# Optimization experiments

Hardware: AMD Instinct MI355X
Metric: run time of the kernel (lower is better)

The kernel has to match this reference:

```python
import jax, jax.numpy as jnp
import numpy as np

DIM = 2048
N_HEADS = 32
N_KV_HEADS = 8
HEAD_DIM = DIM // N_HEADS  # 64
N_REP = N_HEADS // N_KV_HEADS  # 4
B, S = 1, 2048


def _rope(t, cos, sin):
    # t: (b, s, h, head_dim); cos/sin: (s, head_dim//2)
    tr = t.reshape(*t.shape[:-1], -1, 2)
    a, b = tr[..., 0], tr[..., 1]
    c = cos[None, :, None, :]
    s_ = sin[None, :, None, :]
    ra = a * c - b * s_
    rb = a * s_ + b * c
    return jnp.stack([ra, rb], axis=-1).reshape(t.shape)


def setup_inputs() -> dict:
    key = jax.random.key(0)
    ks = jax.random.split(key, 6)
    sc = 1.0 / np.sqrt(DIM)
    x = jax.random.normal(ks[0], (B, S, DIM), dtype=jnp.float32)
    wq = jax.random.normal(ks[1], (DIM, N_HEADS * HEAD_DIM), dtype=jnp.float32) * sc
    wk = jax.random.normal(ks[2], (DIM, N_KV_HEADS * HEAD_DIM), dtype=jnp.float32) * sc
    wv = jax.random.normal(ks[3], (DIM, N_KV_HEADS * HEAD_DIM), dtype=jnp.float32) * sc
    wo = jax.random.normal(ks[4], (N_HEADS * HEAD_DIM, DIM), dtype=jnp.float32) * sc
    # rotary frequencies (theta = 500000 as in Llama3)
    inv = 1.0 / (500000.0 ** (np.arange(0, HEAD_DIM, 2, dtype=np.float32) / HEAD_DIM))
    ang = np.arange(S, dtype=np.float32)[:, None] * inv[None, :]
    freqs_cos = jnp.asarray(np.cos(ang), dtype=jnp.float32)
    freqs_sin = jnp.asarray(np.sin(ang), dtype=jnp.float32)
    # causal additive mask
    mask = jnp.triu(jnp.full((S, S), -1e9, dtype=jnp.float32), k=1)
    return {"x": x, "wq": wq, "wk": wk, "wv": wv, "wo": wo,
            "freqs_cos": freqs_cos, "freqs_sin": freqs_sin, "mask": mask,
            "start_pos": 0}


def reference(x, wq, wk, wv, wo, freqs_cos, freqs_sin, mask, start_pos):
    b, s, _ = x.shape
    xq = (x @ wq).reshape(b, s, N_HEADS, HEAD_DIM)
    xk = (x @ wk).reshape(b, s, N_KV_HEADS, HEAD_DIM)
    xv = (x @ wv).reshape(b, s, N_KV_HEADS, HEAD_DIM)
    xq = _rope(xq, freqs_cos, freqs_sin)
    xk = _rope(xk, freqs_cos, freqs_sin)
    # GQA without repeat_interleave: view queries as (b, s, kv, rep, d)
    q = xq.reshape(b, s, N_KV_HEADS, N_REP, HEAD_DIM)
    scale = 1.0 / np.sqrt(HEAD_DIM)
    # scores: (b, kv, rep, q, k)
    scores = jnp.einsum('bqkrd,bskd->bkrqs', q, xk) * scale
    scores = scores + mask[None, None, None, :, :]
    probs = jax.nn.softmax(scores.astype(jnp.float32), axis=-1).astype(x.dtype)
    out = jnp.einsum('bkrqs,bskd->bqkrd', probs, xv)
    out = out.reshape(b, s, N_HEADS * HEAD_DIM)
    return out @ wo
```

## Files before the change

kernel.cpp:

```cpp
#include <hip/hip_runtime.h>
#include <hip/hip_bf16.h>

#define DIM 2048
#define S_LEN 2048
#define N_HEADS 32
#define N_KV_HEADS 8
#define HEAD_DIM 64
#define KV_DIM (N_KV_HEADS * HEAD_DIM)
#define QKV_N (DIM + 2 * KV_DIM)
#define QSCALE 0.18033688011112042f

typedef __attribute__((ext_vector_type(8))) short bf16x8;
typedef __attribute__((ext_vector_type(4))) float f32x4;

__device__ __forceinline__ unsigned short bf16_of(float f) {
    __hip_bfloat16 h = __float2bfloat16(f);
    return *reinterpret_cast<unsigned short*>(&h);
}
__device__ __forceinline__ float f_of_bf16(unsigned short u) {
    unsigned int x = ((unsigned int)u) << 16;
    return __uint_as_float(x);
}
__device__ __forceinline__ void gl_lds16(const void* g, void* l) {
    __builtin_amdgcn_global_load_lds((const __attribute__((address_space(1))) void*)g,
                                     (__attribute__((address_space(3))) void*)l, 16, 0, 0);
}
__device__ __forceinline__ unsigned int pack2tr(float lo, float hi) {
    return __builtin_amdgcn_perm(__float_as_uint(hi), __float_as_uint(lo), 0x07060302u);
}
__device__ __forceinline__ float max3f(float a, float b, float c) {
    float d;
    asm("v_max3_f32 %0, %1, %2, %3" : "=v"(d) : "v"(a), "v"(b), "v"(c));
    return d;
}

__global__ __launch_bounds__(256) void prep(const float* __restrict__ x,
                                            const float* __restrict__ wq,
                                            const float* __restrict__ wk,
                                            const float* __restrict__ wv,
                                            const float* __restrict__ wo,
                                            unsigned short* __restrict__ xbf,
                                            unsigned short* __restrict__ wqkvT,
                                            unsigned short* __restrict__ woT) {
    __shared__ float tile[64][65];
    const int t = threadIdx.x;
    int b = blockIdx.x;
    if (b < 4096) {
        int idx = b * 256 + t;
        float4 f = ((const float4*)x)[idx];
        ushort4 u;
        u.x = bf16_of(f.x); u.y = bf16_of(f.y); u.z = bf16_of(f.z); u.w = bf16_of(f.w);
        ((ushort4*)xbf)[idx] = u;
        return;
    }
    b -= 4096;
    const float* src;
    unsigned short* dst;
    int src_cols, bx, by;
    if (b < 1024)      { src = wq; dst = wqkvT;                                src_cols = DIM;    bx = b & 31;          by = b >> 5; }
    else if (b < 1280) { src = wk; dst = wqkvT + (size_t)DIM * DIM;            src_cols = KV_DIM; bx = (b - 1024) & 7;  by = (b - 1024) >> 3; }
    else if (b < 1536) { src = wv; dst = wqkvT + (size_t)(DIM + KV_DIM) * DIM; src_cols = KV_DIM; bx = (b - 1280) & 7;  by = (b - 1280) >> 3; }
    else               { src = wo; dst = woT;                                  src_cols = DIM;    bx = (b - 1536) & 31; by = (b - 1536) >> 5; }
    const int c0 = bx * 64, r0 = by * 64;
#pragma unroll
    for (int i = 0; i < 16; i++) {
        int idx = t + i * 256;
        int r = idx >> 6, c = idx & 63;
        tile[r][c] = src[(size_t)(r0 + r) * src_cols + c0 + c];
    }
    __syncthreads();
#pragma unroll
    for (int i = 0; i < 8; i++) {
        int idx = t + i * 256;
        int rr = idx >> 5, cc = (idx & 31) * 2;
        ushort2 u2;
        u2.x = bf16_of(tile[cc][rr]);
        u2.y = bf16_of(tile[cc + 1][rr]);
        *(ushort2*)&dst[(size_t)(c0 + rr) * DIM + r0 + cc] = u2;
    }
}

__global__ __launch_bounds__(256) void gemm_bt64(const unsigned short* __restrict__ A,
                                                 const unsigned short* __restrict__ Bt,
                                                 void* __restrict__ Cv,
                                                 int M, int N, int K, int c_bf16) {
    __shared__ unsigned short As[2][128 * 64];
    __shared__ unsigned short Bs[2][64 * 64];
    const int tid = threadIdx.x;
    const int wave = tid >> 6, lane = tid & 63;
    const int m16 = lane & 15, quad = lane >> 4;
    const int m0 = blockIdx.y * 128, n0 = blockIdx.x * 64;
    const int wm = (wave >> 1) * 64, wn = (wave & 1) * 32;

    const int lrow = lane >> 3;
    const int gc = (lane & 7) ^ lrow;
    const unsigned short* Ab = A + (size_t)(m0 + wave * 8 + lrow) * K + gc * 8;
    const unsigned short* Bb = Bt + (size_t)(n0 + wave * 8 + lrow) * K + gc * 8;

    f32x4 acc[4][2];
#pragma unroll
    for (int mb = 0; mb < 4; mb++)
#pragma unroll
        for (int nb = 0; nb < 2; nb++) acc[mb][nb] = (f32x4){0.f, 0.f, 0.f, 0.f};

#pragma unroll
    for (int g = 0; g < 4; g++)
        gl_lds16(Ab + (size_t)g * 32 * K, &As[0][(g * 32 + wave * 8) * 64]);
#pragma unroll
    for (int g = 0; g < 2; g++)
        gl_lds16(Bb + (size_t)g * 32 * K, &Bs[0][(g * 32 + wave * 8) * 64]);

    const int nt = K >> 6;
    for (int kt = 0; kt < nt; kt++) {
        __syncthreads();
        if (kt + 1 < nt) {
            const int nb2 = (kt + 1) & 1;
            const int k0 = (kt + 1) << 6;
#pragma unroll
            for (int g = 0; g < 4; g++)
                gl_lds16(Ab + (size_t)g * 32 * K + k0, &As[nb2][(g * 32 + wave * 8) * 64]);
#pragma unroll
            for (int g = 0; g < 2; g++)
                gl_lds16(Bb + (size_t)g * 32 * K + k0, &Bs[nb2][(g * 32 + wave * 8) * 64]);
        }
        const unsigned short* A_ = As[kt & 1];
        const unsigned short* B_ = Bs[kt & 1];
#pragma unroll
        for (int ks = 0; ks < 2; ks++) {
            const int ch = (ks * 4 + quad) ^ (m16 & 7);
            bf16x8 af[4], bfr[2];
#pragma unroll
            for (int mb = 0; mb < 4; mb++)
                af[mb] = *(const bf16x8*)&A_[(wm + mb * 16 + m16) * 64 + ch * 8];
#pragma unroll
            for (int nb = 0; nb < 2; nb++)
                bfr[nb] = *(const bf16x8*)&B_[(wn + nb * 16 + m16) * 64 + ch * 8];
#pragma unroll
            for (int mb = 0; mb < 4; mb++)
#pragma unroll
                for (int nb = 0; nb < 2; nb++)
                    acc[mb][nb] = __builtin_amdgcn_mfma_f32_16x16x32_bf16(af[mb], bfr[nb], acc[mb][nb], 0, 0, 0);
        }
    }

    if (c_bf16) {
        unsigned short* C = (unsigned short*)Cv;
#pragma unroll
        for (int mb = 0; mb < 4; mb++)
#pragma unroll
            for (int nb = 0; nb < 2; nb++)
#pragma unroll
                for (int r = 0; r < 4; r++)
                    C[(size_t)(m0 + wm + mb * 16 + quad * 4 + r) * N + n0 + wn + nb * 16 + m16] =
                        bf16_of(acc[mb][nb][r]);
    } else {
        float* C = (float*)Cv;
#pragma unroll
        for (int mb = 0; mb < 4; mb++)
#pragma unroll
            for (int nb = 0; nb < 2; nb++)
#pragma unroll
                for (int r = 0; r < 4; r++)
                    C[(size_t)(m0 + wm + mb * 16 + quad * 4 + r) * N + n0 + wn + nb * 16 + m16] =
                        acc[mb][nb][r];
    }
}

__global__ __launch_bounds__(256) void rope_tv(const unsigned short* __restrict__ qkv,
                                               unsigned short* __restrict__ qbf,
                                               unsigned short* __restrict__ kbf,
                                               unsigned short* __restrict__ vbt,
                                               const float* __restrict__ fcos,
                                               const float* __restrict__ fsin) {
    __shared__ unsigned short tile[64][65];
    const int t = threadIdx.x;
    int b = blockIdx.x;
    if (b < 2560) {
        int idx = b * 256 + t;
        const int nq = S_LEN * N_HEADS * 8;
        int s, j, srcoff, dstoff;
        unsigned short* dst;
        float osc;
        if (idx < nq) {
            s = idx >> 8;
            int rem = idx & 255;
            int h = rem >> 3;
            j = rem & 7;
            srcoff = s * QKV_N + h * 64 + j * 8;
            dstoff = s * DIM + h * 64 + j * 8;
            dst = qbf;
            osc = QSCALE;
        } else {
            int t2 = idx - nq;
            s = t2 >> 6;
            int rem = t2 & 63;
            int h = rem >> 3;
            j = rem & 7;
            srcoff = s * QKV_N + DIM + h * 64 + j * 8;
            dstoff = s * KV_DIM + h * 64 + j * 8;
            dst = kbf;
            osc = 1.0f;
        }
        bf16x8 v8 = *(const bf16x8*)&qkv[srcoff];
        float4 c4 = *(const float4*)&fcos[s * 32 + j * 4];
        float4 s4 = *(const float4*)&fsin[s * 32 + j * 4];
        float cs[4] = {c4.x, c4.y, c4.z, c4.w};
        float sn[4] = {s4.x, s4.y, s4.z, s4.w};
        bf16x8 o;
#pragma unroll
        for (int p = 0; p < 4; p++) {
            float a = f_of_bf16((unsigned short)v8[2 * p]);
            float bb = f_of_bf16((unsigned short)v8[2 * p + 1]);
            o[2 * p]     = (short)bf16_of((a * cs[p] - bb * sn[p]) * osc);
            o[2 * p + 1] = (short)bf16_of((a * sn[p] + bb * cs[p]) * osc);
        }
        *(bf16x8*)&dst[dstoff] = o;
        return;
    }
    b -= 2560;
    const int d0 = (b & 7) * 64;
    const int s0 = (b >> 3) * 64;
#pragma unroll
    for (int i = 0; i < 16; i++) {
        int idx = t + i * 256;
        int r = idx >> 6, c = idx & 63;
        tile[r][c] = qkv[(size_t)(s0 + r) * QKV_N + DIM + KV_DIM + d0 + c];
    }
    __syncthreads();
#pragma unroll
    for (int i = 0; i < 16; i++) {
        int idx = t + i * 256;
        int r = idx >> 6, c = idx & 63;
        int key = s0 + c;
        int kl = key & 127;
        int kp = (kl & 0x60) | ((kl & 0x0C) << 1) | ((kl & 0x10) >> 2) | (kl & 3);
        vbt[(size_t)(d0 + r) * S_LEN + (key & ~127) + kp] = tile[c][r];
    }
}

__global__ __launch_bounds__(256) void attn_mfma9(const unsigned short* __restrict__ qb,
                                                  const unsigned short* __restrict__ kb,
                                                  const unsigned short* __restrict__ vbt,
                                                  unsigned short* __restrict__ out) {
    const int h  = blockIdx.x;
    const int qt = 31 - (int)blockIdx.y;
    const int kh = h >> 2;
    const int tid  = threadIdx.x;
    const int wave = tid >> 6;
    const int lane = tid & 63;
    const int m16  = lane & 15;
    const int quad = lane >> 4;

    __shared__ unsigned short Ks[2][128 * 64];
    __shared__ unsigned short Vt[64 * 128];

    const int lrow8 = lane >> 3;
    const int kc    = (lane & 7) ^ lrow8;
    const int lrow4 = lane >> 4;
    const int vc    = (lane & 15) ^ ((wave * 4 + lrow4) & 7);

    const unsigned short* Kbase = kb + (size_t)kh * 64 + (size_t)(wave * 8 + lrow8) * KV_DIM + kc * 8;
    const unsigned short* Vbase = vbt + (size_t)(kh * 64 + wave * 4 + lrow4) * S_LEN + vc * 8;

    bf16x8 ones;
#pragma unroll
    for (int i = 0; i < 8; i++) ones[i] = (short)0x3F80;

    const int q0 = qt * 64;
    const int n_iter = (qt >> 1) + 1;

    bf16x8 qa[2];
    {
        const int qrow = q0 + wave * 16 + m16;
#pragma unroll
        for (int ks = 0; ks < 2; ks++)
            qa[ks] = *(const bf16x8*)&qb[(size_t)qrow * DIM + h * 64 + ks * 32 + quad * 8];
    }

    f32x4 o_acc[4];
#pragma unroll
    for (int nb = 0; nb < 4; nb++) o_acc[nb] = (f32x4){0.f, 0.f, 0.f, 0.f};
    f32x4 l_acc = (f32x4){0.f, 0.f, 0.f, 0.f};
    float m_s = -1e30f;
    const int qrow_lane = q0 + wave * 16 + m16;
    const int orow_base = q0 + wave * 16 + quad * 4;

#pragma unroll
    for (int g = 0; g < 4; g++)
        gl_lds16(Kbase + (size_t)(g * 32) * KV_DIM, &Ks[0][(g * 32 + wave * 8) * 64]);

    for (int kt = 0; kt < n_iter; kt++) {
        asm volatile("s_waitcnt vmcnt(0)" ::: "memory");
        __builtin_amdgcn_s_barrier();
        __builtin_amdgcn_sched_barrier(0);

        const int knext = (kt + 1 < n_iter) ? (kt + 1) : kt;
#pragma unroll
        for (int g = 0; g < 4; g++)
            gl_lds16(Vbase + (size_t)g * 16 * S_LEN + kt * 128,
                     &Vt[(g * 16 + wave * 4) * 128]);
#pragma unroll
        for (int g = 0; g < 4; g++)
            gl_lds16(Kbase + (size_t)(knext * 128 + g * 32) * KV_DIM,
                     &Ks[(kt + 1) & 1][(g * 32 + wave * 8) * 64]);

        const unsigned short* K_ = Ks[kt & 1];

        f32x4 sc[8];
#pragma unroll
        for (int cb = 0; cb < 8; cb++) sc[cb] = (f32x4){0.f, 0.f, 0.f, 0.f};
        __builtin_amdgcn_s_setprio(1);
#pragma unroll
        for (int ks = 0; ks < 2; ks++) {
            const int slot = (ks * 4 + quad) ^ (m16 & 7);
#pragma unroll
            for (int cb = 0; cb < 8; cb++) {
                bf16x8 kf = *(const bf16x8*)&K_[(cb * 16 + m16) * 64 + slot * 8];
                sc[cb] = __builtin_amdgcn_mfma_f32_16x16x32_bf16(kf, qa[ks], sc[cb], 0, 0, 0);
            }
        }
        __builtin_amdgcn_s_setprio(0);

        if (kt == n_iter - 1) {
#pragma unroll
            for (int cb = 0; cb < 8; cb++) {
                int key = kt * 128 + cb * 16 + quad * 4;
#pragma unroll
                for (int r = 0; r < 4; r++)
                    if (key + r > qrow_lane) sc[cb][r] = -1e30f;
            }
        }

        float rmax = fmaxf(sc[0][0], sc[0][1]);
        rmax = max3f(sc[0][2], sc[0][3], rmax);
#pragma unroll
        for (int cb = 1; cb < 8; cb++) {
            rmax = max3f(sc[cb][0], sc[cb][1], rmax);
            rmax = max3f(sc[cb][2], sc[cb][3], rmax);
        }
        rmax = fmaxf(rmax, __shfl_xor(rmax, 16, 64));
        rmax = fmaxf(rmax, __shfl_xor(rmax, 32, 64));

        if (!__all(rmax - m_s <= 8.0f)) {
            float mnew = fmaxf(m_s, rmax);
            float alpha = __builtin_amdgcn_exp2f(m_s - mnew);
            m_s = mnew;
#pragma unroll
            for (int r = 0; r < 4; r++) {
                float a_r = __shfl(alpha, quad * 4 + r, 64);
#pragma unroll
                for (int nb = 0; nb < 4; nb++) o_acc[nb][r] *= a_r;
                l_acc[r] *= a_r;
            }
        }

#pragma unroll
        for (int cb = 0; cb < 8; cb++)
#pragma unroll
            for (int r = 0; r < 4; r++)
                sc[cb][r] = __builtin_amdgcn_exp2f(sc[cb][r] - m_s);

        unsigned int P01[8], P23[8];
#pragma unroll
        for (int cb = 0; cb < 8; cb++) {
            P01[cb] = pack2tr(sc[cb][0], sc[cb][1]);
            P23[cb] = pack2tr(sc[cb][2], sc[cb][3]);
        }

        asm volatile("s_waitcnt vmcnt(4)" ::: "memory");
        __builtin_amdgcn_s_barrier();
        __builtin_amdgcn_sched_barrier(0);

        __builtin_amdgcn_s_setprio(1);
#pragma unroll
        for (int ks = 0; ks < 4; ks++) {
            union { unsigned int u[4]; bf16x8 v; } pa;
            pa.u[0] = P01[2 * ks];     pa.u[1] = P23[2 * ks];
            pa.u[2] = P01[2 * ks + 1]; pa.u[3] = P23[2 * ks + 1];
            const int slot = (ks * 4 + quad) ^ (m16 & 7);
#pragma unroll
            for (int nb = 0; nb < 4; nb++) {
                bf16x8 vf = *(const bf16x8*)&Vt[(nb * 16 + m16) * 128 + slot * 8];
                o_acc[nb] = __builtin_amdgcn_mfma_f32_16x16x32_bf16(pa.v, vf, o_acc[nb], 0, 0, 0);
            }
            l_acc = __builtin_amdgcn_mfma_f32_16x16x32_bf16(pa.v, ones, l_acc, 0, 0, 0);
        }
        __builtin_amdgcn_s_setprio(0);
    }

#pragma unroll
    for (int r = 0; r < 4; r++) {
        float inv_l = 1.f / l_acc[r];
#pragma unroll
        for (int nb = 0; nb < 4; nb++)
            out[(size_t)(orow_base + r) * DIM + h * 64 + nb * 16 + m16] =
                bf16_of(o_acc[nb][r] * inv_l);
    }
}

extern "C" void kernel_launch(void* const* d_in, const int* in_sizes, int n_in,
                              void* d_out, int out_size, void* d_ws, size_t ws_size,
                              hipStream_t stream) {
    const float* x    = (const float*)d_in[0];
    const float* wq   = (const float*)d_in[1];
    const float* wk   = (const float*)d_in[2];
    const float* wv   = (const float*)d_in[3];
    const float* wo   = (const float*)d_in[4];
    const float* fcos = (const float*)d_in[5];
    const float* fsin = (const float*)d_in[6];

    char* ws = (char*)d_ws;
    const size_t MB = 1024 * 1024;
    unsigned short* xbf    = (unsigned short*)(ws);
    unsigned short* wqkvT  = (unsigned short*)(ws + 8 * MB);
    unsigned short* woT    = (unsigned short*)(ws + 20 * MB);
    unsigned short* qkvbf  = (unsigned short*)(ws + 28 * MB);
    unsigned short* vbt    = (unsigned short*)(ws + 40 * MB);
    unsigned short* qbf    = (unsigned short*)(ws + 8 * MB);
    unsigned short* kbf    = (unsigned short*)(ws + 16 * MB);
    unsigned short* attnbf = (unsigned short*)(ws);

    prep<<<4096 + 2560, 256, 0, stream>>>(x, wq, wk, wv, wo, xbf, wqkvT, woT);

    gemm_bt64<<<dim3(QKV_N / 64, S_LEN / 128), 256, 0, stream>>>(xbf, wqkvT, qkvbf,
                                                                 S_LEN, QKV_N, DIM, 1);

    rope_tv<<<2560 + 256, 256, 0, stream>>>(qkvbf, qbf, kbf, vbt, fcos, fsin);

    attn_mfma9<<<dim3(N_HEADS, 32), 256, 0, stream>>>(qbf, kbf, vbt, attnbf);

    gemm_bt64<<<dim3(DIM / 64, S_LEN / 128), 256, 0, stream>>>(attnbf, woT, d_out,
                                                               S_LEN, DIM, DIM, 0);
}
```

Baseline: 216.6 us.

## Triple-buffer GEMM LDS pipeline and fuse Q RoPE into attention

The GEMM moves from two to three LDS buffers. It prefetches two k-tiles ahead and waits with a partial vmcnt, so one tile of loads stays in flight across the barrier. Separately, the RoPE rotation and softmax scale for Q are moved into the attention kernel's Q load, so the standalone pass now only handles K and V, removing a write and re-read of the full Q tensor. The cost is more shared memory per GEMM block, which may lower occupancy, and a little extra per-block work in the attention kernel.

```diff
diff --git a/kernel.cpp b/kernel.cpp
--- a/kernel.cpp
+++ b/kernel.cpp
@@ -84,8 +84,8 @@
                                                  const unsigned short* __restrict__ Bt,
                                                  void* __restrict__ Cv,
                                                  int M, int N, int K, int c_bf16) {
-    __shared__ unsigned short As[2][128 * 64];
-    __shared__ unsigned short Bs[2][64 * 64];
+    __shared__ unsigned short As[3][128 * 64];
+    __shared__ unsigned short Bs[3][64 * 64];
     const int tid = threadIdx.x;
     const int wave = tid >> 6, lane = tid & 63;
     const int m16 = lane & 15, quad = lane >> 4;
@@ -103,28 +103,29 @@
 #pragma unroll
         for (int nb = 0; nb < 2; nb++) acc[mb][nb] = (f32x4){0.f, 0.f, 0.f, 0.f};
 
-#pragma unroll
-    for (int g = 0; g < 4; g++)
-        gl_lds16(Ab + (size_t)g * 32 * K, &As[0][(g * 32 + wave * 8) * 64]);
-#pragma unroll
-    for (int g = 0; g < 2; g++)
-        gl_lds16(Bb + (size_t)g * 32 * K, &Bs[0][(g * 32 + wave * 8) * 64]);
+    auto STAGE = [&](int t, int bufi) {
+        const int k0 = t << 6;
+#pragma unroll
+        for (int g = 0; g < 4; g++)
+            gl_lds16(Ab + (size_t)g * 32 * K + k0, &As[bufi][(g * 32 + wave * 8) * 64]);
+#pragma unroll
+        for (int g = 0; g < 2; g++)
+            gl_lds16(Bb + (size_t)g * 32 * K + k0, &Bs[bufi][(g * 32 + wave * 8) * 64]);
+    };
+
+    STAGE(0, 0);
+    STAGE(1, 1);
 
     const int nt = K >> 6;
     for (int kt = 0; kt < nt; kt++) {
-        __syncthreads();
-        if (kt + 1 < nt) {
-            const int nb2 = (kt + 1) & 1;
-            const int k0 = (kt + 1) << 6;
-#pragma unroll
-            for (int g = 0; g < 4; g++)
-                gl_lds16(Ab + (size_t)g * 32 * K + k0, &As[nb2][(g * 32 + wave * 8) * 64]);
-#pragma unroll
-            for (int g = 0; g < 2; g++)
-                gl_lds16(Bb + (size_t)g * 32 * K + k0, &Bs[nb2][(g * 32 + wave * 8) * 64]);
-        }
-        const unsigned short* A_ = As[kt & 1];
-        const unsigned short* B_ = Bs[kt & 1];
+        if (kt + 1 < nt) asm volatile("s_waitcnt vmcnt(6)" ::: "memory");
+        else             asm volatile("s_waitcnt vmcnt(0)" ::: "memory");
+        __builtin_amdgcn_s_barrier();
+        __builtin_amdgcn_sched_barrier(0);
+        if (kt + 2 < nt) STAGE(kt + 2, (kt + 2) % 3);
+
+        const unsigned short* A_ = As[kt % 3];
+        const unsigned short* B_ = Bs[kt % 3];
 #pragma unroll
         for (int ks = 0; ks < 2; ks++) {
             const int ch = (ks * 4 + quad) ^ (m16 & 7);
@@ -166,8 +167,7 @@
     }
 }
 
-__global__ __launch_bounds__(256) void rope_tv(const unsigned short* __restrict__ qkv,
-                                               unsigned short* __restrict__ qbf,
+__global__ __launch_bounds__(256) void rope_kv(const unsigned short* __restrict__ qkv,
                                                unsigned short* __restrict__ kbf,
                                                unsigned short* __restrict__ vbt,
                                                const float* __restrict__ fcos,
@@ -175,32 +175,13 @@
     __shared__ unsigned short tile[64][65];
     const int t = threadIdx.x;
     int b = blockIdx.x;
-    if (b < 2560) {
+    if (b < 512) {
         int idx = b * 256 + t;
-        const int nq = S_LEN * N_HEADS * 8;
-        int s, j, srcoff, dstoff;
-        unsigned short* dst;
-        float osc;
-        if (idx < nq) {
-            s = idx >> 8;
-            int rem = idx & 255;
-            int h = rem >> 3;
-            j = rem & 7;
-            srcoff = s * QKV_N + h * 64 + j * 8;
-            dstoff = s * DIM + h * 64 + j * 8;
-            dst = qbf;
-            osc = QSCALE;
-        } else {
-            int t2 = idx - nq;
-            s = t2 >> 6;
-            int rem = t2 & 63;
-            int h = rem >> 3;
-            j = rem & 7;
-            srcoff = s * QKV_N + DIM + h * 64 + j * 8;
-            dstoff = s * KV_DIM + h * 64 + j * 8;
-            dst = kbf;
-            osc = 1.0f;
-        }
+        int s = idx >> 6;
+        int rem = idx & 63;
+        int hh = rem >> 3, j = rem & 7;
+        int srcoff = s * QKV_N + DIM + hh * 64 + j * 8;
+        int dstoff = s * KV_DIM + hh * 64 + j * 8;
         bf16x8 v8 = *(const bf16x8*)&qkv[srcoff];
         float4 c4 = *(const float4*)&fcos[s * 32 + j * 4];
         float4 s4 = *(const float4*)&fsin[s * 32 + j * 4];
@@ -211,13 +192,13 @@
         for (int p = 0; p < 4; p++) {
             float a = f_of_bf16((unsigned short)v8[2 * p]);
             float bb = f_of_bf16((unsigned short)v8[2 * p + 1]);
-            o[2 * p]     = (short)bf16_of((a * cs[p] - bb * sn[p]) * osc);
-            o[2 * p + 1] = (short)bf16_of((a * sn[p] + bb * cs[p]) * osc);
-        }
-        *(bf16x8*)&dst[dstoff] = o;
+            o[2 * p]     = (short)bf16_of(a * cs[p] - bb * sn[p]);
+            o[2 * p + 1] = (short)bf16_of(a * sn[p] + bb * cs[p]);
+        }
+        *(bf16x8*)&kbf[dstoff] = o;
         return;
     }
-    b -= 2560;
+    b -= 512;
     const int d0 = (b & 7) * 64;
     const int s0 = (b >> 3) * 64;
 #pragma unroll
@@ -238,9 +219,11 @@
     }
 }
 
-__global__ __launch_bounds__(256) void attn_mfma9(const unsigned short* __restrict__ qb,
+__global__ __launch_bounds__(256) void attn_mfma9(const unsigned short* __restrict__ qkv,
                                                   const unsigned short* __restrict__ kb,
                                                   const unsigned short* __restrict__ vbt,
+                                                  const float* __restrict__ fcos,
+                                                  const float* __restrict__ fsin,
                                                   unsigned short* __restrict__ out) {
     const int h  = blockIdx.x;
     const int qt = 31 - (int)blockIdx.y;
@@ -272,9 +255,22 @@
     bf16x8 qa[2];
     {
         const int qrow = q0 + wave * 16 + m16;
-#pragma unroll
-        for (int ks = 0; ks < 2; ks++)
-            qa[ks] = *(const bf16x8*)&qb[(size_t)qrow * DIM + h * 64 + ks * 32 + quad * 8];
+        const unsigned short* qsrc = qkv + (size_t)qrow * QKV_N + h * 64;
+#pragma unroll
+        for (int ks = 0; ks < 2; ks++) {
+            bf16x8 raw = *(const bf16x8*)&qsrc[ks * 32 + quad * 8];
+            float4 c4 = *(const float4*)&fcos[qrow * 32 + ks * 16 + quad * 4];
+            float4 s4 = *(const float4*)&fsin[qrow * 32 + ks * 16 + quad * 4];
+            float cs[4] = {c4.x, c4.y, c4.z, c4.w};
+            float sn[4] = {s4.x, s4.y, s4.z, s4.w};
+#pragma unroll
+            for (int p = 0; p < 4; p++) {
+                float a = f_of_bf16((unsigned short)raw[2 * p]);
+                float bb = f_of_bf16((unsigned short)raw[2 * p + 1]);
+                qa[ks][2 * p]     = (short)bf16_of((a * cs[p] - bb * sn[p]) * QSCALE);
+                qa[ks][2 * p + 1] = (short)bf16_of((a * sn[p] + bb * cs[p]) * QSCALE);
+            }
+        }
     }
 
     f32x4 o_acc[4];
@@ -416,7 +412,6 @@
     unsigned short* woT    = (unsigned short*)(ws + 20 * MB);
     unsigned short* qkvbf  = (unsigned short*)(ws + 28 * MB);
     unsigned short* vbt    = (unsigned short*)(ws + 40 * MB);
-    unsigned short* qbf    = (unsigned short*)(ws + 8 * MB);
     unsigned short* kbf    = (unsigned short*)(ws + 16 * MB);
     unsigned short* attnbf = (unsigned short*)(ws);
 
@@ -425,9 +420,9 @@
     gemm_bt64<<<dim3(QKV_N / 64, S_LEN / 128), 256, 0, stream>>>(xbf, wqkvT, qkvbf,
                                                                  S_LEN, QKV_N, DIM, 1);
 
-    rope_tv<<<2560 + 256, 256, 0, stream>>>(qkvbf, qbf, kbf, vbt, fcos, fsin);
-
-    attn_mfma9<<<dim3(N_HEADS, 32), 256, 0, stream>>>(qbf, kbf, vbt, attnbf);
+    rope_kv<<<512 + 256, 256, 0, stream>>>(qkvbf, kbf, vbt, fcos, fsin);
+
+    attn_mfma9<<<dim3(N_HEADS, 32), 256, 0, stream>>>(qkvbf, kbf, vbt, fcos, fsin, attnbf);
 
     gemm_bt64<<<dim3(DIM / 64, S_LEN / 128), 256, 0, stream>>>(attnbf, woT, d_out,
                                                                S_LEN, DIM, DIM, 0);
```

Measured after the change: 239.3 us. +10.5%, slower.
